# Optimization experiments

Measured on AMD Instinct MI355X. Metric: run time of the kernel, lower is better.

Reference implementation:

```python
import jax, jax.numpy as jnp
import numpy as np

B, S, D, H, HD = 4, 2048, 768, 12, 64
P = H * HD
LR = 0.1

def _ln(x, g, b, eps=1e-5):
    m = jnp.mean(x, axis=-1, keepdims=True)
    v = jnp.mean((x - m) ** 2, axis=-1, keepdims=True)
    return (x - m) / jnp.sqrt(v + eps) * g + b

def _modifier(x, w1, b1, w2, b2):
    # Linear -> GELU(exact) -> Linear, matching nn.Sequential(Linear, GELU, Linear)
    h = jax.nn.gelu(x @ w1.T + b1, approximate=False)
    return h @ w2.T + b2

def setup_inputs() -> dict:
    key = jax.random.key(0)
    ks = jax.random.split(key, 16)
    def n(k, shape, s=0.02):
        return jax.random.normal(k, shape, jnp.float32) * s
    inp = {}
    inp['x'] = jax.random.normal(ks[0], (B, S, D), jnp.float32)
    inp['ln_in_g'] = jnp.ones((D,), jnp.float32)
    inp['ln_in_b'] = jnp.zeros((D,), jnp.float32)
    inp['Wk'] = n(ks[1], (P, D))
    inp['Wv'] = n(ks[2], (P, D))
    inp['Wq'] = n(ks[3], (P, D))
    inp['km_w1'] = n(ks[4], (D // 4, D), 0.01); inp['km_b1'] = jnp.zeros((D // 4,), jnp.float32)
    inp['km_w2'] = n(ks[5], (P, D // 4), 0.01); inp['km_b2'] = jnp.zeros((P,), jnp.float32)
    inp['vm_w1'] = n(ks[6], (D // 4, D), 0.01); inp['vm_b1'] = jnp.zeros((D // 4,), jnp.float32)
    inp['vm_w2'] = n(ks[7], (P, D // 4), 0.01); inp['vm_b2'] = jnp.zeros((P,), jnp.float32)
    inp['qm_w1'] = n(ks[8], (D // 4, D), 0.01); inp['qm_b1'] = jnp.zeros((D // 4,), jnp.float32)
    inp['qm_w2'] = n(ks[9], (P, D // 4), 0.01); inp['qm_b2'] = jnp.zeros((P,), jnp.float32)
    inp['lnk_g'] = jnp.ones((HD,), jnp.float32); inp['lnk_b'] = jnp.zeros((HD,), jnp.float32)
    inp['lnv_g'] = jnp.ones((HD,), jnp.float32); inp['lnv_b'] = jnp.zeros((HD,), jnp.float32)
    inp['lnq_g'] = jnp.ones((HD,), jnp.float32); inp['lnq_b'] = jnp.zeros((HD,), jnp.float32)
    inp['Wo'] = n(ks[10], (D, P))
    inp['lr_scale'] = jnp.ones((H,), jnp.float32)
    inp['Wg'] = n(ks[11], (D, D))
    inp['bg'] = jnp.zeros((D,), jnp.float32)
    return inp

def reference(x, ln_in_g, ln_in_b, Wk, Wv, Wq,
              km_w1, km_b1, km_w2, km_b2,
              vm_w1, vm_b1, vm_w2, vm_b2,
              qm_w1, qm_b1, qm_w2, qm_b2,
              lnk_g, lnk_b, lnv_g, lnv_b, lnq_g, lnq_b,
              Wo, lr_scale, Wg, bg):
    b, s, d = x.shape
    xn = _ln(x, ln_in_g, ln_in_b)  # norm_input
    # data-dependent projections (context defaults to x_normed)
    k = xn @ Wk.T + 0.1 * _modifier(xn, km_w1, km_b1, km_w2, km_b2)
    v = xn @ Wv.T + 0.1 * _modifier(xn, vm_w1, vm_b1, vm_w2, vm_b2)
    q = xn @ Wq.T + 0.1 * _modifier(xn, qm_w1, qm_b1, qm_w2, qm_b2)
    k = _ln(k.reshape(b, s, H, HD), lnk_g, lnk_b)
    v = _ln(v.reshape(b, s, H, HD), lnv_g, lnv_b)
    q = _ln(q.reshape(b, s, H, HD), lnq_g, lnq_b)
    # scan over time: (s, b, h, d)
    k_s = jnp.transpose(k, (1, 0, 2, 3))
    v_s = jnp.transpose(v, (1, 0, 2, 3))
    q_s = jnp.transpose(q, (1, 0, 2, 3))
    lr = jax.nn.sigmoid(lr_scale) * LR * 2.0  # (H,)
    M0 = jnp.zeros((b, H, HD, HD), x.dtype)

    def step(M, kvq):
        k_t, v_t, q_t = kvq  # each (b, h, d)
        out_t = jnp.einsum('bhdk,bhk->bhd', M, q_t)  # read before update
        kn = k_t / (jnp.linalg.norm(k_t, axis=-1, keepdims=True) + 1e-6)
        pred = jnp.einsum('bhdk,bhk->bhd', M, kn)
        surprise = pred - v_t
        # M - outer(pred, kn) - lr * outer(surprise, kn), fused
        coef = pred + lr[None, :, None] * surprise  # (b, h, d)
        M_new = M - jnp.einsum('bhd,bhk->bhdk', coef, kn)
        return M_new, out_t

    M_final, outs = jax.lax.scan(step, M0, (k_s, v_s, q_s))  # outs: (s, b, h, d)
    out = jnp.transpose(outs, (1, 0, 2, 3)).reshape(b, s, H * HD)
    out = out @ Wo.T
    gate = jax.nn.sigmoid(x @ Wg.T + bg)  # output_gate on raw x
    out = gate * out
    return out, M_final
```

## Files before the change

### kernel.cpp

```cpp
#include <hip/hip_runtime.h>
#include <hip/hip_bf16.h>
#include <math.h>

#define B_ 4
#define S_ 2048
#define D_ 768
#define H_ 12
#define HD_ 64
#define P_ 768
#define M_ (B_*S_)
#define NCH 32
#define CH 64
#define BH (B_*H_)

typedef __hip_bfloat16 bf16;
typedef __attribute__((ext_vector_type(8))) short short8;
typedef __attribute__((ext_vector_type(4))) short s16x4;
typedef __attribute__((ext_vector_type(4))) float f32x4;

__device__ __forceinline__ float wave_reduce_sum(float v){
  #pragma unroll
  for (int off=32; off>0; off>>=1) v += __shfl_xor(v, off, 64);
  return v;
}
__device__ __forceinline__ float bf2f(bf16 h){ return __bfloat162float(h); }
__device__ __forceinline__ float us2f(unsigned short u){
  union{unsigned int i; float f;} z; z.i = ((unsigned int)u)<<16; return z.f;
}
__device__ __forceinline__ int adr(int row, int col){ return (row*128 + col*2) ^ ((row&7)<<4); }
__device__ __forceinline__ short8 lfrag(const char* base, int row, int col){
  return *(const short8*)(base + adr(row,col));
}
__device__ __forceinline__ short8 gfrag(const bf16* g, int row, int col){
  return *(const short8*)(g + row*64 + col);
}
__device__ __forceinline__ f32x4 MM(short8 a, short8 b, f32x4 c){
  return __builtin_amdgcn_mfma_f32_16x16x32_bf16(a, b, c, 0,0,0);
}
__device__ __forceinline__ short f2s(float v){ bf16 h = __float2bfloat16(v); return *(short*)&h; }
__device__ __forceinline__ void stpk(char* b, int n, int m0, float v0,float v1,float v2,float v3){
  s16x4 p = { f2s(v0), f2s(v1), f2s(v2), f2s(v3) };
  *(s16x4*)(b + adr(n, m0)) = p;
}
__device__ __forceinline__ void stpk_hl(char* bh, char* bl, int n, int m0,
                                        float v0,float v1,float v2,float v3){
  float h0=bf2f(__float2bfloat16(v0)), h1=bf2f(__float2bfloat16(v1));
  float h2=bf2f(__float2bfloat16(v2)), h3=bf2f(__float2bfloat16(v3));
  stpk(bh, n, m0, h0,h1,h2,h3);
  stpk(bl, n, m0, v0-h0, v1-h1, v2-h2, v3-h3);
}
__device__ __forceinline__ float4 ldpk2(const char* bh, const char* bl, int n, int m0){
  s16x4 a = *(const s16x4*)(bh + adr(n,m0));
  s16x4 b = *(const s16x4*)(bl + adr(n,m0));
  return make_float4(us2f((unsigned short)a[0])+us2f((unsigned short)b[0]),
                     us2f((unsigned short)a[1])+us2f((unsigned short)b[1]),
                     us2f((unsigned short)a[2])+us2f((unsigned short)b[2]),
                     us2f((unsigned short)a[3])+us2f((unsigned short)b[3]));
}
__device__ __forceinline__ void gl_lds(const bf16* g, const bf16* l){
  __builtin_amdgcn_global_load_lds(
      (const __attribute__((address_space(1))) void*)g,
      (__attribute__((address_space(3))) void*)l, 16, 0, 0);
}

__global__ __launch_bounds__(256) void pack_all_kernel(
    const float* __restrict__ km1,const float* __restrict__ vm1,const float* __restrict__ qm1,
    const float* __restrict__ Wk,const float* __restrict__ Wv,const float* __restrict__ Wq,
    const float* __restrict__ k2,const float* __restrict__ v2,const float* __restrict__ q2,
    const float* __restrict__ Wo,const float* __restrict__ Wg,
    const float* __restrict__ kb1,const float* __restrict__ vb1,const float* __restrict__ qb1,
    const float* __restrict__ kb2,const float* __restrict__ vb2,const float* __restrict__ qb2,
    const float* __restrict__ lnkg,const float* __restrict__ lnvg,const float* __restrict__ lnqg,
    const float* __restrict__ lnkb,const float* __restrict__ lnvb,const float* __restrict__ lnqb,
    bf16* __restrict__ Whb, bf16* __restrict__ Wkvqb, bf16* __restrict__ Wob,
    bf16* __restrict__ Wgb, float* __restrict__ biasb)
{
  int i = blockIdx.x*256 + threadIdx.x;
  if (i < 491520){
    int r = i/768, c = i%768;
    float v = 0.f;
    if (r < 192) v = km1[r*768+c];
    else if (r < 384) v = vm1[(r-192)*768+c];
    else if (r < 576) v = qm1[(r-384)*768+c];
    Whb[i] = __float2bfloat16(v);
  } else if (i < 2703360){
    int i2 = i - 491520;
    int r = i2/960, c = i2%960;
    int p = r/768, rr = r%768;
    const float* W  = (p==0)?Wk:(p==1)?Wv:Wq;
    const float* w2 = (p==0)?k2:(p==1)?v2:q2;
    float v = (c < 768) ? W[(size_t)rr*768+c] : 0.1f*w2[(size_t)rr*192 + (c-768)];
    Wkvqb[i2] = __float2bfloat16(v);
  } else if (i < 3293184){
    int i2 = i - 2703360;
    Wob[i2] = __float2bfloat16(Wo[i2]);
  } else if (i < 3883008){
    int i2 = i - 3293184;
    Wgb[i2] = __float2bfloat16(Wg[i2]);
  } else if (i < 3886272){
    int i2 = i - 3883008;
    if (i2 < 576){
      biasb[i2] = (i2<192)? kb1[i2] : (i2<384)? vb1[i2-192] : qb1[i2-384];
    } else if (i2 < 2880){
      int r = i2-576; int p = r/768, rr = r%768;
      const float* b2 = (p==0)?kb2:(p==1)?vb2:qb2;
      biasb[i2] = 0.1f*b2[rr];
    } else if (i2 < 3072){
      int k3 = i2-2880; int gg=k3/64, cc=k3%64;
      biasb[i2] = (gg==0?lnkg:gg==1?lnvg:lnqg)[cc];
    } else {
      int k3 = i2-3072; int gg=k3/64, cc=k3%64;
      biasb[i2] = (gg==0?lnkb:gg==1?lnvb:lnqb)[cc];
    }
  }
}

__global__ __launch_bounds__(256) void ln_in_kernel(const float* __restrict__ x, const float* __restrict__ g,
                                                    const float* __restrict__ bta,
                                                    bf16* __restrict__ xn, bf16* __restrict__ xb){
  int row = blockIdx.x;
  const float* xr = x + (size_t)row*D_;
  int t = threadIdx.x;
  float v0 = xr[t], v1 = xr[t+256], v2 = xr[t+512];
  float s  = v0+v1+v2;
  float sq = v0*v0+v1*v1+v2*v2;
  s = wave_reduce_sum(s); sq = wave_reduce_sum(sq);
  __shared__ float red[8];
  int w = t>>6;
  if ((t&63)==0){ red[w]=s; red[4+w]=sq; }
  __syncthreads();
  s  = red[0]+red[1]+red[2]+red[3];
  sq = red[4]+red[5]+red[6]+red[7];
  float mean = s*(1.f/D_);
  float var  = sq*(1.f/D_) - mean*mean;
  float inv  = rsqrtf(var + 1e-5f);
  bf16* xnr = xn + (size_t)row*D_;
  bf16* xbr = xb + (size_t)row*D_;
  xnr[t]     = __float2bfloat16((v0-mean)*inv*g[t]     + bta[t]);
  xnr[t+256] = __float2bfloat16((v1-mean)*inv*g[t+256] + bta[t+256]);
  xnr[t+512] = __float2bfloat16((v2-mean)*inv*g[t+512] + bta[t+512]);
  xbr[t] = __float2bfloat16(v0); xbr[t+256] = __float2bfloat16(v1); xbr[t+512] = __float2bfloat16(v2);
}

template<int MODE>
__global__ __launch_bounds__(256) void gemm_kernel(
    const bf16* __restrict__ A1, int lda1, int K1,
    const bf16* __restrict__ A2, int lda2, int K2, int a2_gstride,
    const bf16* __restrict__ Bw, int ldb, int ngroup,
    const float* __restrict__ bias, const float* __restrict__ extra,
    const float* __restrict__ lng, const float* __restrict__ lnb,
    void* __restrict__ outp, int Nout)
{
  __shared__ bf16 Asm[2][128*64];
  __shared__ bf16 Bsm[2][128*64];
  const int t = threadIdx.x;
  const int w = t>>6, L = t&63;
  const int m0 = blockIdx.x*128, n0 = blockIdx.y*128;
  const int g = blockIdx.z;
  const int wm = w>>1, wn = w&1;
  const int Ktot = K1 + K2;
  const int nk = Ktot >> 6;

  const int srow_base = w*32 + (L>>3);
  const int scol = ((L&7) ^ ((L>>3)&7))*8;

  int aoff[4][2], boff[4][2];
  #pragma unroll
  for (int f=0;f<4;f++){
    int arow = wm*64 + f*16 + (L&15);
    int brow = wn*64 + f*16 + (L&15);
    #pragma unroll
    for (int q=0;q<2;q++){
      int slot = q*4 + (L>>4);
      aoff[f][q] = arow*64 + ((slot ^ (arow&7))*8);
      boff[f][q] = brow*64 + ((slot ^ (brow&7))*8);
    }
  }

  const bf16* BrowBase = Bw + (size_t)(g*ngroup + n0)*ldb;

  auto STAGE = [&](int buf, int k0){
    const bf16* Ab; int lda; int acol;
    if (k0 < K1){ Ab = A1; lda = lda1; acol = k0 + scol; }
    else        { Ab = A2; lda = lda2; acol = (k0-K1) + g*a2_gstride + scol; }
    #pragma unroll
    for (int i=0;i<4;i++){
      int row = srow_base + i*8;
      gl_lds(Ab + (size_t)(m0+row)*lda + acol,       &Asm[buf][w*2048 + i*512]);
      gl_lds(BrowBase + (size_t)row*ldb + k0 + scol, &Bsm[buf][w*2048 + i*512]);
    }
  };

  f32x4 acc[4][4];
  #pragma unroll
  for (int i=0;i<4;i++)
    #pragma unroll
    for (int j=0;j<4;j++) acc[i][j] = (f32x4){0.f,0.f,0.f,0.f};

  STAGE(0, 0);
  int cur = 0;
  for (int kt=0; kt<nk; ++kt){
    asm volatile("s_waitcnt vmcnt(0)" ::: "memory");
    __syncthreads();
    if (kt+1 < nk) STAGE(cur^1, (kt+1)<<6);
    const bf16* As = Asm[cur];
    const bf16* Bs = Bsm[cur];
    #pragma unroll
    for (int q=0;q<2;q++){
      short8 af[4], bfr[4];
      #pragma unroll
      for (int f=0;f<4;f++){
        af[f]  = *(const short8*)&As[aoff[f][q]];
        bfr[f] = *(const short8*)&Bs[boff[f][q]];
      }
      #pragma unroll
      for (int i=0;i<4;i++)
        #pragma unroll
        for (int j=0;j<4;j++)
          acc[i][j] = MM(af[i], bfr[j], acc[i][j]);
    }
    cur ^= 1;
  }

  if (MODE==1){
    float gco[4], bco[4];
    #pragma unroll
    for (int j=0;j<4;j++){ int cc = j*16 + (L&15); gco[j] = lng[g*64+cc]; bco[j] = lnb[g*64+cc]; }
    #pragma unroll
    for (int i=0;i<4;i++){
      #pragma unroll
      for (int r=0;r<4;r++){
        float v[4];
        #pragma unroll
        for (int j=0;j<4;j++){
          int n = n0 + wn*64 + j*16 + (L&15);
          v[j] = acc[i][j][r] + bias[g*768 + n];
        }
        float s1 = v[0]+v[1]+v[2]+v[3];
        float s2 = v[0]*v[0]+v[1]*v[1]+v[2]*v[2]+v[3]*v[3];
        #pragma unroll
        for (int mk=1; mk<16; mk<<=1){ s1 += __shfl_xor(s1, mk, 64); s2 += __shfl_xor(s2, mk, 64); }
        float mean = s1*(1.f/64.f);
        float var  = s2*(1.f/64.f) - mean*mean;
        float inv  = rsqrtf(var + 1e-5f);
        float y[4];
        #pragma unroll
        for (int j=0;j<4;j++) y[j] = (v[j]-mean)*inv*gco[j] + bco[j];
        if (g==0){
          float n2 = y[0]*y[0]+y[1]*y[1]+y[2]*y[2]+y[3]*y[3];
          #pragma unroll
          for (int mk=1; mk<16; mk<<=1) n2 += __shfl_xor(n2, mk, 64);
          float sc = 1.f/(sqrtf(n2)+1e-6f);
          #pragma unroll
          for (int j=0;j<4;j++) y[j] *= sc;
        }
        int m = m0 + wm*64 + i*16 + (L>>4)*4 + r;
        int b_ = m>>11, s_ = m&2047;
        #pragma unroll
        for (int j=0;j<4;j++){
          int n = n0 + wn*64 + j*16 + (L&15);
          int h_ = n>>6, hd = n&63;
          ((bf16*)outp)[((((size_t)g*B_ + b_)*H_ + h_)*S_ + s_)*HD_ + hd] = __float2bfloat16(y[j]);
        }
      }
    }
  } else {
    #pragma unroll
    for (int i=0;i<4;i++){
      #pragma unroll
      for (int j=0;j<4;j++){
        #pragma unroll
        for (int r=0;r<4;r++){
          int m = m0 + wm*64 + i*16 + (L>>4)*4 + r;
          int n = n0 + wn*64 + j*16 + (L&15);
          float val = acc[i][j][r];
          if (MODE==0){
            if (n < Nout){
              val += bias[n];
              float ge = 0.5f*val*(1.f + erff(val*0.70710678f));
              ((bf16*)outp)[(size_t)m*Nout + n] = __float2bfloat16(ge);
            }
          } else if (MODE==2){
            ((float*)outp)[(size_t)m*Nout + n] = val;
          } else {
            float g2 = extra[(size_t)m*768 + n] + bias[n];
            float gate = 1.f/(1.f + __expf(-g2));
            ((float*)outp)[(size_t)m*Nout + n] = val * gate;
          }
        }
      }
    }
  }
}

__global__ __launch_bounds__(256) void prep_kernel(
    const bf16* __restrict__ kvqb, const float* __restrict__ lr_scale,
    bf16* __restrict__ WKng, bf16* __restrict__ WVTg,
    bf16* __restrict__ AcThi, bf16* __restrict__ AcTlo, bf16* __restrict__ Bcb)
{
  __shared__ __align__(16) char T1[8192];
  __shared__ __align__(16) char T2[8192];
  __shared__ __align__(16) char T3[8192];
  __shared__ __align__(16) char T4[8192];
  __shared__ __align__(16) char T5[8192];

  const int c = blockIdx.x, bh = blockIdx.y;
  const int h = bh % H_;
  const int t = threadIdx.x, w = t>>6, L = t&63;
  const size_t PS = (size_t)B_*H_*S_*HD_;
  const size_t base_k = (size_t)bh*S_*HD_ + (size_t)c*CH*HD_;
  const float lr = 0.2f/(1.f + __expf(-lr_scale[h]));
  const float beta = 1.f + lr;
  const size_t cb = ((size_t)bh*NCH + c)*4096;
  const bf16* Kg = kvqb + base_k;
  const bf16* Vg = kvqb + PS + base_k;

  const int fr = L&15, fc = (L>>4)*8;
  const int m0 = 16*w + (L>>4)*4;
  const int nb = L&15;

  {
    short8 aK[2];
    #pragma unroll
    for (int kk=0;kk<2;kk++) aK[kk] = gfrag(Kg, 16*w+fr, kk*32+fc);
    #pragma unroll
    for (int nt=0;nt<4;nt++){
      f32x4 g = (f32x4){0.f,0.f,0.f,0.f};
      #pragma unroll
      for (int kk=0;kk<2;kk++) g = MM(aK[kk], gfrag(Kg, 16*nt+fr, kk*32+fc), g);
      int n = 16*nt + nb;
      float pv[4], ptv[4], tv[4];
      #pragma unroll
      for (int r=0;r<4;r++){
        int m = m0 + r;
        float val = beta*g[r];
        pv[r]  = (n>m)? val : 0.f;
        ptv[r] = (m>n)? val : 0.f;
        tv[r]  = ((n==m)?1.f:0.f) - pv[r];
      }
      stpk(T3, n, m0, pv[0],pv[1],pv[2],pv[3]);
      stpk(T4, n, m0, ptv[0],ptv[1],ptv[2],ptv[3]);
      stpk_hl(T1, T2, n, m0, tv[0],tv[1],tv[2],tv[3]);
    }
  }
  __syncthreads();

  #pragma unroll
  for (int s=0; s<6; ++s){
    const bool do_upd = (s>=1), do_sq = (s<=4);
    f32x4 upd[4], c1[4], c2[4];
    float4 tr[4];
    short8 aPT[2];
    #pragma unroll
    for (int kk=0;kk<2;kk++) aPT[kk] = lfrag(T4, 16*w+fr, kk*32+fc);
    if (do_upd){
      short8 b1[4][2], b2[4][2];
      #pragma unroll
      for (int nt=0;nt<4;nt++){
        #pragma unroll
        for (int kk=0;kk<2;kk++){
          b1[nt][kk] = lfrag(T1, 16*nt+fr, kk*32+fc);
          b2[nt][kk] = lfrag(T2, 16*nt+fr, kk*32+fc);
        }
        upd[nt] = (f32x4){0.f,0.f,0.f,0.f};
      }
      #pragma unroll
      for (int nt=0;nt<4;nt++)
        #pragma unroll
        for (int kk=0;kk<2;kk++){
          upd[nt] = MM(aPT[kk], b1[nt][kk], upd[nt]);
          upd[nt] = MM(aPT[kk], b2[nt][kk], upd[nt]);
        }
      #pragma unroll
      for (int nt=0;nt<4;nt++) tr[nt] = ldpk2(T1, T2, 16*nt+nb, m0);
    }
    if (do_sq){
      short8 aP[2], bPT[4][2], bP[4][2];
      #pragma unroll
      for (int kk=0;kk<2;kk++) aP[kk] = lfrag(T3, 16*w+fr, kk*32+fc);
      #pragma unroll
      for (int nt=0;nt<4;nt++){
        #pragma unroll
        for (int kk=0;kk<2;kk++){
          bPT[nt][kk] = lfrag(T4, 16*nt+fr, kk*32+fc);
          bP[nt][kk]  = lfrag(T3, 16*nt+fr, kk*32+fc);
        }
        c1[nt] = (f32x4){0.f,0.f,0.f,0.f};
        c2[nt] = (f32x4){0.f,0.f,0.f,0.f};
      }
      #pragma unroll
      for (int nt=0;nt<4;nt++)
        #pragma unroll
        for (int kk=0;kk<2;kk++){
          c1[nt] = MM(aP[kk],  bPT[nt][kk], c1[nt]);
          c2[nt] = MM(aPT[kk], bP[nt][kk],  c2[nt]);
        }
    }
    __syncthreads();
    if (do_upd){
      #pragma unroll
      for (int nt=0;nt<4;nt++){
        int n = 16*nt + nb;
        stpk_hl(T1, T2, n, m0, tr[nt].x+upd[nt][0], tr[nt].y+upd[nt][1],
                               tr[nt].z+upd[nt][2], tr[nt].w+upd[nt][3]);
      }
    }
    if (do_sq){
      #pragma unroll
      for (int nt=0;nt<4;nt++){
        int n = 16*nt + nb;
        stpk(T4, n, m0, c1[nt][0],c1[nt][1],c1[nt][2],c1[nt][3]);
        stpk(T3, n, m0, c2[nt][0],c2[nt][1],c2[nt][2],c2[nt][3]);
      }
    }
    __syncthreads();
  }

  {
    short8 aKg[2], aVg[2];
    #pragma unroll
    for (int kk=0;kk<2;kk++){
      aKg[kk] = gfrag(Kg, 16*w+fr, kk*32+fc);
      aVg[kk] = gfrag(Vg, 16*w+fr, kk*32+fc);
    }
    #pragma unroll
    for (int nt=0;nt<4;nt++){
      f32x4 ck = (f32x4){0.f,0.f,0.f,0.f};
      f32x4 cv = (f32x4){0.f,0.f,0.f,0.f};
      int row = 16*nt + nb;
      #pragma unroll
      for (int kk=0;kk<2;kk++){
        short8 bi;
        int col0 = kk*32 + fc;
        #pragma unroll
        for (int e=0;e<8;e++) bi[e] = (col0+e == 16*nt+fr) ? (short)0x3F80 : (short)0;
        ck = MM(aKg[kk], bi, ck);
        cv = MM(aVg[kk], bi, cv);
      }
      stpk(T3, row, m0, ck[0],ck[1],ck[2],ck[3]);
      stpk(T4, row, m0, cv[0],cv[1],cv[2],cv[3]);
    }
  }
  __syncthreads();

  {
    short8 a1[2], a2[2];
    #pragma unroll
    for (int kk=0;kk<2;kk++){
      a1[kk] = lfrag(T1, 16*w+fr, kk*32+fc);
      a2[kk] = lfrag(T2, 16*w+fr, kk*32+fc);
    }
    f32x4 cwv[4], cwk[4];
    #pragma unroll
    for (int nt=0;nt<4;nt++){ cwv[nt]=(f32x4){0.f,0.f,0.f,0.f}; cwk[nt]=(f32x4){0.f,0.f,0.f,0.f}; }
    #pragma unroll
    for (int nt=0;nt<4;nt++)
      #pragma unroll
      for (int kk=0;kk<2;kk++){
        short8 bV = lfrag(T4, 16*nt+fr, kk*32+fc);
        cwv[nt] = MM(a1[kk], bV, cwv[nt]);
        cwv[nt] = MM(a2[kk], bV, cwv[nt]);
      }
    #pragma unroll
    for (int nt=0;nt<4;nt++)
      #pragma unroll
      for (int kk=0;kk<2;kk++){
        short8 bK = lfrag(T3, 16*nt+fr, kk*32+fc);
        cwk[nt] = MM(a1[kk], bK, cwk[nt]);
        cwk[nt] = MM(a2[kk], bK, cwk[nt]);
      }
    __syncthreads();
    #pragma unroll
    for (int nt=0;nt<4;nt++){
      int n = 16*nt + nb;
      stpk(T5, n, m0, cwv[nt][0],cwv[nt][1],cwv[nt][2],cwv[nt][3]);
      stpk(T4, n, m0, cwk[nt][0],cwk[nt][1],cwk[nt][2],cwk[nt][3]);
    }
  }
  __syncthreads();

  {
    int row = t>>2, seg = (t&3)*16;
    size_t go = cb + (size_t)row*64 + seg;
    *(short8*)(WVTg+go)   = *(const short8*)(T5 + adr(row,seg));
    *(short8*)(WVTg+go+8) = *(const short8*)(T5 + adr(row,seg+8));

    short8 aK2[2], aWKT[2];
    #pragma unroll
    for (int kk=0;kk<2;kk++){
      aK2[kk]  = lfrag(T3, 16*w+fr, kk*32+fc);
      aWKT[kk] = lfrag(T4, 16*w+fr, kk*32+fc);
    }
    f32x4 cBc[4], cWK[4], cAc[4];
    #pragma unroll
    for (int nt=0;nt<4;nt++){ cBc[nt]=(f32x4){0.f,0.f,0.f,0.f}; cWK[nt]=(f32x4){0.f,0.f,0.f,0.f}; cAc[nt]=(f32x4){0.f,0.f,0.f,0.f}; }
    #pragma unroll
    for (int nt=0;nt<4;nt++)
      #pragma unroll
      for (int kk=0;kk<2;kk++){
        short8 bWVT = lfrag(T5, 16*nt+fr, kk*32+fc);
        cBc[nt] = MM(aK2[kk], bWVT, cBc[nt]);
      }
    #pragma unroll
    for (int nt=0;nt<4;nt++)
      #pragma unroll
      for (int kk=0;kk<2;kk++){
        short8 b1 = lfrag(T1, 16*nt+fr, kk*32+fc);
        short8 b2 = lfrag(T2, 16*nt+fr, kk*32+fc);
        cWK[nt] = MM(aK2[kk], b1, cWK[nt]);
        cWK[nt] = MM(aK2[kk], b2, cWK[nt]);
      }
    #pragma unroll
    for (int nt=0;nt<4;nt++)
      #pragma unroll
      for (int kk=0;kk<2;kk++){
        short8 bK3 = lfrag(T3, 16*nt+fr, kk*32+fc);
        cAc[nt] = MM(aWKT[kk], bK3, cAc[nt]);
      }
    __syncthreads();
    #pragma unroll
    for (int nt=0;nt<4;nt++){
      int n = 16*nt + nb;
      stpk(T5, n, m0, lr*cBc[nt][0], lr*cBc[nt][1], lr*cBc[nt][2], lr*cBc[nt][3]);
      stpk(T3, n, m0, cWK[nt][0],cWK[nt][1],cWK[nt][2],cWK[nt][3]);
      float av[4];
      #pragma unroll
      for (int r=0;r<4;r++) av[r] = ((n==m0+r)?1.f:0.f) - beta*cAc[nt][r];
      stpk_hl(T1, T2, n, m0, av[0],av[1],av[2],av[3]);
    }
  }
  __syncthreads();

  {
    int row = t>>2, seg = (t&3)*16;
    size_t go = cb + (size_t)row*64 + seg;
    *(short8*)(AcThi+go)   = *(const short8*)(T1 + adr(row,seg));
    *(short8*)(AcThi+go+8) = *(const short8*)(T1 + adr(row,seg+8));
    *(short8*)(AcTlo+go)   = *(const short8*)(T2 + adr(row,seg));
    *(short8*)(AcTlo+go+8) = *(const short8*)(T2 + adr(row,seg+8));
    *(short8*)(Bcb+go)     = *(const short8*)(T5 + adr(row,seg));
    *(short8*)(Bcb+go+8)   = *(const short8*)(T5 + adr(row,seg+8));
    *(short8*)(WKng+go)    = *(const short8*)(T3 + adr(row,seg));
    *(short8*)(WKng+go+8)  = *(const short8*)(T3 + adr(row,seg+8));
  }
}

__global__ __launch_bounds__(256) void seq_kernel(
    const bf16* __restrict__ AcThi, const bf16* __restrict__ AcTlo,
    const bf16* __restrict__ Bcb,
    bf16* __restrict__ Mpref, float* __restrict__ Mout)
{
  __shared__ __align__(16) char sM[4][2][2048];
  const int bh = blockIdx.x;
  const int t = threadIdx.x, w = t>>6, L = t&63;
  char* mhi = sM[w][0]; char* mlo = sM[w][1];
  const size_t cbase = (size_t)bh*NCH*4096;

  { float4 z = {0.f,0.f,0.f,0.f};
    #pragma unroll
    for (int i=0;i<2;i++){ ((float4*)mhi)[L + 64*i] = z; ((float4*)mlo)[L + 64*i] = z; } }
  { short8 z = {0,0,0,0,0,0,0,0};
    #pragma unroll
    for (int i=0;i<2;i++) ((short8*)(Mpref + cbase))[t + 256*i] = z; }

  short8 Xbh[4][2], Xbl[4][2]; float Xbc[4][4];
  short8 Ybh[4][2], Ybl[4][2]; float Ybc[4][4];

  auto loadf = [&](short8 (&fbh)[4][2], short8 (&fbl)[4][2], float (&fbc)[4][4], int c){
    size_t cb = cbase + (size_t)c*4096;
    #pragma unroll
    for (int nt=0;nt<4;nt++){
      #pragma unroll
      for (int kk=0;kk<2;kk++){
        size_t o = cb + (size_t)(16*nt + (L&15))*64 + kk*32 + (L>>4)*8;
        fbh[nt][kk] = *(const short8*)(AcThi + o);
        fbl[nt][kk] = *(const short8*)(AcTlo + o);
      }
      #pragma unroll
      for (int r=0;r<4;r++)
        fbc[nt][r] = us2f(*(const unsigned short*)(Bcb + cb + (size_t)(16*w + (L>>4)*4 + r)*64 + nt*16 + (L&15)));
    }
  };
  auto compute = [&](short8 (&fbh)[4][2], short8 (&fbl)[4][2], float (&fbc)[4][4], int c){
    short8 ah[2], al[2];
    #pragma unroll
    for (int kk=0;kk<2;kk++){
      ah[kk] = lfrag(mhi, L&15, kk*32 + (L>>4)*8);
      al[kk] = lfrag(mlo, L&15, kk*32 + (L>>4)*8);
    }
    #pragma unroll
    for (int nt=0;nt<4;nt++){
      f32x4 acc = { fbc[nt][0], fbc[nt][1], fbc[nt][2], fbc[nt][3] };
      acc = MM(ah[0], fbh[nt][0], acc);
      acc = MM(ah[1], fbh[nt][1], acc);
      acc = MM(ah[0], fbl[nt][0], acc);
      acc = MM(ah[1], fbl[nt][1], acc);
      acc = MM(al[0], fbh[nt][0], acc);
      acc = MM(al[1], fbh[nt][1], acc);
      #pragma unroll
      for (int r=0;r<4;r++){
        float f = acc[r];
        bf16 hi = __float2bfloat16(f);
        int lrow = (L>>4)*4 + r, col = nt*16 + (L&15);
        int off = ((lrow*128 + col*2) ^ ((lrow&7)<<4));
        *(bf16*)(mhi + off) = hi;
        *(bf16*)(mlo + off) = __float2bfloat16(f - bf2f(hi));
        if (c < NCH-1)
          Mpref[cbase + (size_t)(c+1)*4096 + (size_t)(16*w + lrow)*64 + col] = hi;
        else
          Mout[((size_t)bh*64 + 16*w + lrow)*64 + col] = f;
      }
    }
  };

  loadf(Xbh,Xbl,Xbc,0);
  for (int c=0;c<NCH;c+=2){
    loadf(Ybh,Ybl,Ybc,c+1);
    compute(Xbh,Xbl,Xbc,c);
    if (c+2 < NCH) loadf(Xbh,Xbl,Xbc,c+2);
    compute(Ybh,Ybl,Ybc,c+1);
  }
}

__global__ __launch_bounds__(256) void outphase_kernel(
    const bf16* __restrict__ kvqb, const bf16* __restrict__ Mpref,
    const bf16* __restrict__ WKng, const bf16* __restrict__ WVTb,
    const float* __restrict__ lr_scale, bf16* __restrict__ attn)
{
  __shared__ __align__(16) char sUT[8192];
  __shared__ __align__(16) char sAT[8192];
  const int c = blockIdx.x, bh = blockIdx.y;
  const int b = bh / H_, h = bh % H_;
  const int t = threadIdx.x, w = t>>6, L = t&63;
  const size_t PS = (size_t)B_*H_*S_*HD_;
  const size_t cb = ((size_t)bh*NCH + c)*4096;
  const size_t base_k = (size_t)bh*S_*HD_ + (size_t)c*CH*HD_;
  const bf16* Kg = kvqb + base_k;
  const bf16* Qg = kvqb + 2*PS + base_k;
  const float lr = 0.2f/(1.f + __expf(-lr_scale[h]));
  const float beta = 1.f + lr;
  const int fr = L&15, fc = (L>>4)*8;
  const int m0 = 16*w + (L>>4)*4;
  const int nb = L&15;

  {
    short8 aKn[2];
    #pragma unroll
    for (int kk=0;kk<2;kk++) aKn[kk] = gfrag(Kg, 16*w+fr, kk*32+fc);
    #pragma unroll
    for (int nt=0;nt<4;nt++){
      f32x4 cat = (f32x4){0.f,0.f,0.f,0.f};
      #pragma unroll
      for (int kk=0;kk<2;kk++) cat = MM(aKn[kk], gfrag(Qg, 16*nt+fr, kk*32+fc), cat);
      int n = 16*nt + nb;
      float v[4];
      #pragma unroll
      for (int r=0;r<4;r++) v[r] = (m0+r < n)? cat[r] : 0.f;
      stpk(sAT, n, m0, v[0],v[1],v[2],v[3]);
    }
  }

  short8 mb[4][2], qa[2], wa[2];
  #pragma unroll
  for (int kk=0;kk<2;kk++){
    qa[kk] = gfrag(Qg, 16*w+fr, kk*32+fc);
    wa[kk] = *(const short8*)(WKng + cb + (size_t)(16*w + fr)*64 + kk*32 + fc);
  }
  #pragma unroll
  for (int nt=0;nt<4;nt++)
    #pragma unroll
    for (int kk=0;kk<2;kk++)
      mb[nt][kk] = *(const short8*)(Mpref + cb + (size_t)(16*nt + fr)*64 + kk*32 + fc);
  f32x4 aout[4], ap[4];
  #pragma unroll
  for (int nt=0;nt<4;nt++){ aout[nt]=(f32x4){0.f,0.f,0.f,0.f}; ap[nt]=(f32x4){0.f,0.f,0.f,0.f}; }
  #pragma unroll
  for (int nt=0;nt<4;nt++)
    #pragma unroll
    for (int kk=0;kk<2;kk++){
      aout[nt] = MM(qa[kk], mb[nt][kk], aout[nt]);
      ap[nt]   = MM(wa[kk], mb[nt][kk], ap[nt]);
    }
  #pragma unroll
  for (int nt=0;nt<4;nt++){
    s16x4 wv4 = *(const s16x4*)(WVTb + cb + (size_t)(nt*16 + (L&15))*64 + 16*w + (L>>4)*4);
    short us[4];
    #pragma unroll
    for (int r=0;r<4;r++){
      float wv = us2f((unsigned short)wv4[r]);
      us[r] = f2s(lr*wv - beta*ap[nt][r]);
    }
    int d = nt*16 + (L&15);
    int i0 = 16*w + (L>>4)*4;
    s16x4 pk = { us[0], us[1], us[2], us[3] };
    *(s16x4*)(sUT + adr(d, i0)) = pk;
  }
  __syncthreads();
  short8 ta[2], ub[4][2];
  #pragma unroll
  for (int kk=0;kk<2;kk++)
    ta[kk] = lfrag(sAT, 16*w+fr, kk*32+fc);
  #pragma unroll
  for (int nt=0;nt<4;nt++)
    #pragma unroll
    for (int kk=0;kk<2;kk++)
      ub[nt][kk] = lfrag(sUT, 16*nt + fr, kk*32 + fc);
  #pragma unroll
  for (int nt=0;nt<4;nt++)
    #pragma unroll
    for (int kk=0;kk<2;kk++)
      aout[nt] = MM(ta[kk], ub[nt][kk], aout[nt]);
  #pragma unroll
  for (int nt=0;nt<4;nt++)
    #pragma unroll
    for (int r=0;r<4;r++)
      attn[((size_t)b*S_ + (size_t)c*CH + 16*w + (L>>4)*4 + r)*P_ + h*HD_ + nt*16 + (L&15)]
        = __float2bfloat16(aout[nt][r]);
}

extern "C" void kernel_launch(void* const* d_in, const int* in_sizes, int n_in,
                              void* d_out, int out_size, void* d_ws, size_t ws_size,
                              hipStream_t stream)
{
  const float* x     = (const float*)d_in[0];
  const float* ln_g  = (const float*)d_in[1];
  const float* ln_b  = (const float*)d_in[2];
  const float* Wk    = (const float*)d_in[3];
  const float* Wv    = (const float*)d_in[4];
  const float* Wq    = (const float*)d_in[5];
  const float* km_w1 = (const float*)d_in[6];  const float* km_b1 = (const float*)d_in[7];
  const float* km_w2 = (const float*)d_in[8];  const float* km_b2 = (const float*)d_in[9];
  const float* vm_w1 = (const float*)d_in[10]; const float* vm_b1 = (const float*)d_in[11];
  const float* vm_w2 = (const float*)d_in[12]; const float* vm_b2 = (const float*)d_in[13];
  const float* qm_w1 = (const float*)d_in[14]; const float* qm_b1 = (const float*)d_in[15];
  const float* qm_w2 = (const float*)d_in[16]; const float* qm_b2 = (const float*)d_in[17];
  const float* lnk_g = (const float*)d_in[18]; const float* lnk_b = (const float*)d_in[19];
  const float* lnv_g = (const float*)d_in[20]; const float* lnv_b = (const float*)d_in[21];
  const float* lnq_g = (const float*)d_in[22]; const float* lnq_b = (const float*)d_in[23];
  const float* Wo    = (const float*)d_in[24];
  const float* lr_sc = (const float*)d_in[25];
  const float* Wg    = (const float*)d_in[26];
  const float* bg    = (const float*)d_in[27];

  const size_t CHB = (size_t)BH*NCH*4096;

  char* ws = (char*)d_ws;
  size_t o = 0;
  bf16* xnb   = (bf16*)(ws + o); o += (size_t)M_*D_*2;
  bf16* xb    = (bf16*)(ws + o); o += (size_t)M_*D_*2;
  bf16* Hb    = (bf16*)(ws + o); o += (size_t)M_*576*2;
  bf16* kvqb  = (bf16*)(ws + o); o += (size_t)3*M_*P_*2;
  bf16* attn  = (bf16*)(ws + o); o += (size_t)M_*P_*2;
  size_t o_p = o;
  bf16* AcThi = (bf16*)(ws + o); o += CHB*2;
  bf16* AcTlo = (bf16*)(ws + o); o += CHB*2;
  bf16* Bcb   = (bf16*)(ws + o); o += CHB*2;
  bf16* WVTb  = (bf16*)(ws + o); o += CHB*2;
  bf16* WKng  = (bf16*)(ws + o); o += CHB*2;
  bf16* Mpref = (bf16*)(ws + o); o += CHB*2;
  bf16* Whb   = (bf16*)(ws + o); o += (size_t)640*768*2;
  bf16* Wkvqb = (bf16*)(ws + o); o += (size_t)2304*960*2;
  bf16* Wob   = (bf16*)(ws + o); o += (size_t)768*768*2;
  bf16* Wgb   = (bf16*)(ws + o); o += (size_t)768*768*2;
  float* biasb= (float*)(ws + o); o += 3264*4;
  float* G2   = (float*)(ws + o_p);

  float* outF = (float*)d_out;
  float* Mout = outF + (size_t)M_*D_;

  pack_all_kernel<<<15181, 256, 0, stream>>>(
      km_w1, vm_w1, qm_w1, Wk, Wv, Wq, km_w2, vm_w2, qm_w2, Wo, Wg,
      km_b1, vm_b1, qm_b1, km_b2, vm_b2, qm_b2,
      lnk_g, lnv_g, lnq_g, lnk_b, lnv_b, lnq_b,
      Whb, Wkvqb, Wob, Wgb, biasb);

  ln_in_kernel<<<M_, 256, 0, stream>>>(x, ln_g, ln_b, xnb, xb);

  gemm_kernel<0><<<dim3(64,5,1), 256, 0, stream>>>(xnb, 768, 768, nullptr, 0, 0, 0,
                                                   Whb, 768, 640, biasb, nullptr, nullptr, nullptr, Hb, 576);
  gemm_kernel<1><<<dim3(64,6,3), 256, 0, stream>>>(xnb, 768, 768, Hb, 576, 192, 192,
                                                   Wkvqb, 960, 768, biasb + 576, nullptr,
                                                   biasb + 2880, biasb + 3072, kvqb, 768);

  prep_kernel<<<dim3(NCH, BH), 256, 0, stream>>>(kvqb, lr_sc, WKng, WVTb, AcThi, AcTlo, Bcb);
  seq_kernel<<<BH, 256, 0, stream>>>(AcThi, AcTlo, Bcb, Mpref, Mout);
  outphase_kernel<<<dim3(NCH, BH), 256, 0, stream>>>(kvqb, Mpref, WKng, WVTb, lr_sc, attn);

  gemm_kernel<2><<<dim3(64,6,1), 256, 0, stream>>>(xb, 768, 768, nullptr, 0, 0, 0,
                                                   Wgb, 768, 768, nullptr, nullptr, nullptr, nullptr, G2, 768);
  gemm_kernel<3><<<dim3(64,6,1), 256, 0, stream>>>(attn, 768, 768, nullptr, 0, 0, 0,
                                                   Wob, 768, 768, bg, G2, nullptr, nullptr, outF, 768);
}
```

Baseline: 286.5 us.

## Triple-buffer GEMM with K=32 tiles and add bf16 low-part state to outphase

The GEMM kernel moves from a double-buffered 64-wide K tile to a three-stage ring of 32-wide K tiles. It waits with a partial vmcnt so two tile loads stay in flight while the current tile is computed, which should hide global-load latency better. Separately, the sequential kernel now also writes the bf16 low residual of the chunk-prefix state, and the outphase kernel uses both parts in its MFMAs. That raises accuracy but doubles the prefix-state traffic and the outphase MFMA work.

```diff
diff --git a/kernel.cpp b/kernel.cpp
--- a/kernel.cpp
+++ b/kernel.cpp
@@ -151,43 +151,39 @@
     const float* __restrict__ lng, const float* __restrict__ lnb,
     void* __restrict__ outp, int Nout)
 {
-  __shared__ bf16 Asm[2][128*64];
-  __shared__ bf16 Bsm[2][128*64];
+  __shared__ bf16 Asm[3][128*32];
+  __shared__ bf16 Bsm[3][128*32];
   const int t = threadIdx.x;
   const int w = t>>6, L = t&63;
   const int m0 = blockIdx.x*128, n0 = blockIdx.y*128;
   const int g = blockIdx.z;
   const int wm = w>>1, wn = w&1;
   const int Ktot = K1 + K2;
-  const int nk = Ktot >> 6;
-
-  const int srow_base = w*32 + (L>>3);
-  const int scol = ((L&7) ^ ((L>>3)&7))*8;
-
-  int aoff[4][2], boff[4][2];
+  const int nk = Ktot >> 5;
+
+  const int srow = L>>2;
+  const int scol8 = ((L&3) ^ ((L>>2)&3))*8;
+
+  int aoff[4], boff[4];
   #pragma unroll
   for (int f=0;f<4;f++){
     int arow = wm*64 + f*16 + (L&15);
     int brow = wn*64 + f*16 + (L&15);
-    #pragma unroll
-    for (int q=0;q<2;q++){
-      int slot = q*4 + (L>>4);
-      aoff[f][q] = arow*64 + ((slot ^ (arow&7))*8);
-      boff[f][q] = brow*64 + ((slot ^ (brow&7))*8);
-    }
+    aoff[f] = arow*32 + (((L>>4) ^ (arow&3))<<3);
+    boff[f] = brow*32 + (((L>>4) ^ (brow&3))<<3);
   }
 
   const bf16* BrowBase = Bw + (size_t)(g*ngroup + n0)*ldb;
 
   auto STAGE = [&](int buf, int k0){
     const bf16* Ab; int lda; int acol;
-    if (k0 < K1){ Ab = A1; lda = lda1; acol = k0 + scol; }
-    else        { Ab = A2; lda = lda2; acol = (k0-K1) + g*a2_gstride + scol; }
-    #pragma unroll
-    for (int i=0;i<4;i++){
-      int row = srow_base + i*8;
-      gl_lds(Ab + (size_t)(m0+row)*lda + acol,       &Asm[buf][w*2048 + i*512]);
-      gl_lds(BrowBase + (size_t)row*ldb + k0 + scol, &Bsm[buf][w*2048 + i*512]);
+    if (k0 < K1){ Ab = A1; lda = lda1; acol = k0 + scol8; }
+    else        { Ab = A2; lda = lda2; acol = (k0-K1) + g*a2_gstride + scol8; }
+    #pragma unroll
+    for (int i=0;i<2;i++){
+      int row = w*32 + i*16 + srow;
+      gl_lds(Ab + (size_t)(m0+row)*lda + acol,         &Asm[buf][w*1024 + i*512]);
+      gl_lds(BrowBase + (size_t)row*ldb + k0 + scol8,  &Bsm[buf][w*1024 + i*512]);
     }
   };
 
@@ -198,28 +194,32 @@
     for (int j=0;j<4;j++) acc[i][j] = (f32x4){0.f,0.f,0.f,0.f};
 
   STAGE(0, 0);
-  int cur = 0;
+  STAGE(1, 32);
+  int rd = 0;
   for (int kt=0; kt<nk; ++kt){
-    asm volatile("s_waitcnt vmcnt(0)" ::: "memory");
-    __syncthreads();
-    if (kt+1 < nk) STAGE(cur^1, (kt+1)<<6);
-    const bf16* As = Asm[cur];
-    const bf16* Bs = Bsm[cur];
-    #pragma unroll
-    for (int q=0;q<2;q++){
-      short8 af[4], bfr[4];
-      #pragma unroll
-      for (int f=0;f<4;f++){
-        af[f]  = *(const short8*)&As[aoff[f][q]];
-        bfr[f] = *(const short8*)&Bs[boff[f][q]];
-      }
-      #pragma unroll
-      for (int i=0;i<4;i++)
-        #pragma unroll
-        for (int j=0;j<4;j++)
-          acc[i][j] = MM(af[i], bfr[j], acc[i][j]);
-    }
-    cur ^= 1;
+    if (kt == nk-1) asm volatile("s_waitcnt vmcnt(0)" ::: "memory");
+    else            asm volatile("s_waitcnt vmcnt(4)" ::: "memory");
+    asm volatile("s_waitcnt lgkmcnt(0)" ::: "memory");
+    __builtin_amdgcn_s_barrier();
+    __builtin_amdgcn_sched_barrier(0);
+    if (kt+2 < nk){
+      int st = rd+2; if (st>=3) st-=3;
+      STAGE(st, (kt+2)<<5);
+    }
+    const bf16* As = Asm[rd];
+    const bf16* Bs = Bsm[rd];
+    short8 af[4], bfr[4];
+    #pragma unroll
+    for (int f=0;f<4;f++){
+      af[f]  = *(const short8*)&As[aoff[f]];
+      bfr[f] = *(const short8*)&Bs[boff[f]];
+    }
+    #pragma unroll
+    for (int i=0;i<4;i++)
+      #pragma unroll
+      for (int j=0;j<4;j++)
+        acc[i][j] = MM(af[i], bfr[j], acc[i][j]);
+    rd = (rd==2)?0:rd+1;
   }
 
   if (MODE==1){
@@ -548,7 +548,7 @@
 __global__ __launch_bounds__(256) void seq_kernel(
     const bf16* __restrict__ AcThi, const bf16* __restrict__ AcTlo,
     const bf16* __restrict__ Bcb,
-    bf16* __restrict__ Mpref, float* __restrict__ Mout)
+    bf16* __restrict__ Mpref, bf16* __restrict__ Mplo, float* __restrict__ Mout)
 {
   __shared__ __align__(16) char sM[4][2][2048];
   const int bh = blockIdx.x;
@@ -561,7 +561,10 @@
     for (int i=0;i<2;i++){ ((float4*)mhi)[L + 64*i] = z; ((float4*)mlo)[L + 64*i] = z; } }
   { short8 z = {0,0,0,0,0,0,0,0};
     #pragma unroll
-    for (int i=0;i<2;i++) ((short8*)(Mpref + cbase))[t + 256*i] = z; }
+    for (int i=0;i<2;i++){
+      ((short8*)(Mpref + cbase))[t + 256*i] = z;
+      ((short8*)(Mplo  + cbase))[t + 256*i] = z;
+    } }
 
   short8 Xbh[4][2], Xbl[4][2]; float Xbc[4][4];
   short8 Ybh[4][2], Ybl[4][2]; float Ybc[4][4];
@@ -601,14 +604,18 @@
       for (int r=0;r<4;r++){
         float f = acc[r];
         bf16 hi = __float2bfloat16(f);
+        float lo = f - bf2f(hi);
         int lrow = (L>>4)*4 + r, col = nt*16 + (L&15);
         int off = ((lrow*128 + col*2) ^ ((lrow&7)<<4));
         *(bf16*)(mhi + off) = hi;
-        *(bf16*)(mlo + off) = __float2bfloat16(f - bf2f(hi));
-        if (c < NCH-1)
-          Mpref[cbase + (size_t)(c+1)*4096 + (size_t)(16*w + lrow)*64 + col] = hi;
-        else
+        *(bf16*)(mlo + off) = __float2bfloat16(lo);
+        if (c < NCH-1){
+          size_t go = cbase + (size_t)(c+1)*4096 + (size_t)(16*w + lrow)*64 + col;
+          Mpref[go] = hi;
+          Mplo[go]  = __float2bfloat16(lo);
+        } else {
           Mout[((size_t)bh*64 + 16*w + lrow)*64 + col] = f;
+        }
       }
     }
   };
@@ -623,7 +630,7 @@
 }
 
 __global__ __launch_bounds__(256) void outphase_kernel(
-    const bf16* __restrict__ kvqb, const bf16* __restrict__ Mpref,
+    const bf16* __restrict__ kvqb, const bf16* __restrict__ Mpref, const bf16* __restrict__ Mplo,
     const bf16* __restrict__ WKng, const bf16* __restrict__ WVTb,
     const float* __restrict__ lr_scale, bf16* __restrict__ attn)
 {
@@ -660,7 +667,7 @@
     }
   }
 
-  short8 mb[4][2], qa[2], wa[2];
+  short8 mbh[4][2], mbl[4][2], qa[2], wa[2];
   #pragma unroll
   for (int kk=0;kk<2;kk++){
     qa[kk] = gfrag(Qg, 16*w+fr, kk*32+fc);
@@ -669,8 +676,11 @@
   #pragma unroll
   for (int nt=0;nt<4;nt++)
     #pragma unroll
-    for (int kk=0;kk<2;kk++)
-      mb[nt][kk] = *(const short8*)(Mpref + cb + (size_t)(16*nt + fr)*64 + kk*32 + fc);
+    for (int kk=0;kk<2;kk++){
+      size_t o = cb + (size_t)(16*nt + fr)*64 + kk*32 + fc;
+      mbh[nt][kk] = *(const short8*)(Mpref + o);
+      mbl[nt][kk] = *(const short8*)(Mplo  + o);
+    }
   f32x4 aout[4], ap[4];
   #pragma unroll
   for (int nt=0;nt<4;nt++){ aout[nt]=(f32x4){0.f,0.f,0.f,0.f}; ap[nt]=(f32x4){0.f,0.f,0.f,0.f}; }
@@ -678,8 +688,10 @@
   for (int nt=0;nt<4;nt++)
     #pragma unroll
     for (int kk=0;kk<2;kk++){
-      aout[nt] = MM(qa[kk], mb[nt][kk], aout[nt]);
-      ap[nt]   = MM(wa[kk], mb[nt][kk], ap[nt]);
+      aout[nt] = MM(qa[kk], mbh[nt][kk], aout[nt]);
+      aout[nt] = MM(qa[kk], mbl[nt][kk], aout[nt]);
+      ap[nt]   = MM(wa[kk], mbh[nt][kk], ap[nt]);
+      ap[nt]   = MM(wa[kk], mbl[nt][kk], ap[nt]);
     }
   #pragma unroll
   for (int nt=0;nt<4;nt++){
@@ -758,6 +770,7 @@
   bf16* WVTb  = (bf16*)(ws + o); o += CHB*2;
   bf16* WKng  = (bf16*)(ws + o); o += CHB*2;
   bf16* Mpref = (bf16*)(ws + o); o += CHB*2;
+  bf16* Mplo  = (bf16*)(ws + o); o += CHB*2;
   bf16* Whb   = (bf16*)(ws + o); o += (size_t)640*768*2;
   bf16* Wkvqb = (bf16*)(ws + o); o += (size_t)2304*960*2;
   bf16* Wob   = (bf16*)(ws + o); o += (size_t)768*768*2;
@@ -783,8 +796,8 @@
                                                    biasb + 2880, biasb + 3072, kvqb, 768);
 
   prep_kernel<<<dim3(NCH, BH), 256, 0, stream>>>(kvqb, lr_sc, WKng, WVTb, AcThi, AcTlo, Bcb);
-  seq_kernel<<<BH, 256, 0, stream>>>(AcThi, AcTlo, Bcb, Mpref, Mout);
-  outphase_kernel<<<dim3(NCH, BH), 256, 0, stream>>>(kvqb, Mpref, WKng, WVTb, lr_sc, attn);
+  seq_kernel<<<BH, 256, 0, stream>>>(AcThi, AcTlo, Bcb, Mpref, Mplo, Mout);
+  outphase_kernel<<<dim3(NCH, BH), 256, 0, stream>>>(kvqb, Mpref, Mplo, WKng, WVTb, lr_sc, attn);
 
   gemm_kernel<2><<<dim3(64,6,1), 256, 0, stream>>>(xb, 768, 768, nullptr, 0, 0, 0,
                                                    Wgb, 768, 768, nullptr, nullptr, nullptr, nullptr, G2, 768);
```

After: 306.9 us. 1.07x slower.
